# Performance work log

Measured on AMD Instinct MI355X. Metric: run time of the kernel, lower is better.

## Reference

```python
import jax, jax.numpy as jnp
import numpy as np

N, M, D = 500000, 128, 16

def setup_inputs() -> dict:
    key = jax.random.key(0)
    k1, k2, k3 = jax.random.split(key, 3)
    points = jax.random.uniform(k1, (N, D), dtype=jnp.float32)
    centers = jax.random.uniform(k2, (M, D), dtype=jnp.float32)
    # module initializes covs_inv_sqrt = 15*I per center; add small noise so it's non-trivial
    covs_inv_sqrt = 15.0 * jnp.eye(D, dtype=jnp.float32)[None, :, :] \
        + 0.1 * jax.random.normal(k3, (M, D, D), dtype=jnp.float32)
    weights = jnp.ones((M,), dtype=jnp.float32)
    threshold = jnp.zeros((1,), dtype=jnp.float32)
    return {"points": points, "centers": centers, "covs_inv_sqrt": covs_inv_sqrt,
            "weights": weights, "threshold": threshold}

def reference(points, centers, covs_inv_sqrt, weights, threshold):
    # refresh(): covs_inv = L @ L^T per center
    covs_inv = jnp.einsum('jde,jfe->jdf', covs_inv_sqrt, covs_inv_sqrt)  # [M,D,D]
    # equal_clusters=True branch
    w = jnp.abs(weights)
    center_prs = w / (w.sum() + 1e-30)
    coefs = center_prs * jnp.sqrt(jnp.linalg.det(covs_inv))  # [M]
    # Mahalanobis quadratic form (x-c)^T S (x-c) expanded as xSx - 2 xSc + cSc
    S_flat = covs_inv.reshape(M, D * D)                          # [M,D^2]
    xx = (points[:, :, None] * points[:, None, :]).reshape(-1, D * D)  # [N,D^2]
    Sc = jnp.einsum('jde,je->jd', covs_inv, centers)             # [M,D]
    cSc = jnp.einsum('jd,jd->j', centers, Sc)                    # [M]
    q = xx @ S_flat.T - 2.0 * (points @ Sc.T) + cSc[None, :]     # [N,M]
    d_ij = -0.5 * q
    # weighted online logsumexp over centers (KeOps logsumexp with weight Vj(coefs))
    log_lik = jax.nn.logsumexp(d_ij, axis=1, b=coefs[None, :], keepdims=True)  # [N,1]
    return log_lik - threshold
```

## Files before the change

kernel.cpp:

```cpp
#include <hip/hip_runtime.h>
#include <math.h>

#define M_CTR 128
#define D_DIM 16
#define KSTEPS 10
#define NSLOT 80
#define GRID_MAIN 4096
#define WS_CONST_F32_OFF 10240
#define LOG2E 1.4426950408889634f
#define LN2   0.6931471805599453f

typedef _Float16 half8 __attribute__((ext_vector_type(8)));
typedef float f32x16 __attribute__((ext_vector_type(16)));

struct SlotTab { unsigned char a[NSLOT]; unsigned char b[NSLOT]; unsigned char m[NSLOT]; };
constexpr SlotTab make_tab() {
    SlotTab T{};
    int s = 0;
    for (int d = 0; d < 8; ++d) { T.a[s] = (unsigned char)d; T.b[s] = (unsigned char)d; T.m[s] = 0; ++s; }
    for (int d = 0; d < 8; ++d)
        for (int f = d + 1; f < 8; ++f) { T.a[s] = (unsigned char)d; T.b[s] = (unsigned char)f; T.m[s] = 0; ++s; }
    for (int d = 0; d < 8; ++d)
        for (int f2 = d + 1; f2 < 8; ++f2) { T.a[s] = (unsigned char)d; T.b[s] = (unsigned char)(f2 + 8); T.m[s] = 0; ++s; }
    for (int d = 0; d < 4; ++d) { T.a[s] = (unsigned char)d; T.b[s] = (unsigned char)(d + 8); T.m[s] = 1; ++s; }
    for (int d = 0; d < 8; ++d) { T.a[s] = (unsigned char)d; T.b[s] = 0; T.m[s] = 2; ++s; }
    for (; s < NSLOT; ++s) { T.a[s] = 0; T.b[s] = 0; T.m[s] = 3; }
    return T;
}
constexpr SlotTab TAB = make_tab();

__global__ __launch_bounds__(64) void gmm_prep_kernel(
    const float* __restrict__ centers,
    const float* __restrict__ Lmat,
    const float* __restrict__ weights,
    float* __restrict__ ws)
{
    const int j    = blockIdx.x;
    const int lane = threadIdx.x;
    const int r    = lane & 15;

    __shared__ float S_lds[D_DIM][D_DIM + 1];
    __shared__ float Scp_lds[D_DIM];

    float Lr[D_DIM];
    {
        const float4* Lrow = (const float4*)(Lmat + (size_t)j * 256 + r * 16);
        #pragma unroll
        for (int q = 0; q < 4; ++q) {
            const float4 v = Lrow[q];
            Lr[q * 4 + 0] = v.x; Lr[q * 4 + 1] = v.y;
            Lr[q * 4 + 2] = v.z; Lr[q * 4 + 3] = v.w;
        }
    }

    float u[D_DIM];
    #pragma unroll
    for (int e = 0; e < D_DIM; ++e) u[e] = Lr[e];
    float logdet = 0.f;
    #pragma unroll
    for (int k = 0; k < D_DIM; ++k) {
        const float pk = __shfl(u[k], k);
        logdet += logf(fabsf(pk));
        const float f = u[k] * (1.0f / pk);
        #pragma unroll
        for (int c = k + 1; c < D_DIM; ++c) {
            const float rkc = __shfl(u[c], k);
            if (r > k) u[c] -= f * rkc;
        }
    }

    #pragma unroll
    for (int f = 0; f < D_DIM; ++f) {
        float acc = 0.f;
        #pragma unroll
        for (int e = 0; e < D_DIM; ++e) acc += Lr[e] * __shfl(Lr[e], f);
        if (lane < D_DIM) S_lds[lane][f] = acc;
    }
    __syncthreads();

    float c[D_DIM];
    {
        const float4* cc = (const float4*)(centers + (size_t)j * D_DIM);
        #pragma unroll
        for (int q = 0; q < 4; ++q) {
            const float4 v = cc[q];
            c[q * 4 + 0] = v.x - 0.5f; c[q * 4 + 1] = v.y - 0.5f;
            c[q * 4 + 2] = v.z - 0.5f; c[q * 4 + 3] = v.w - 0.5f;
        }
    }
    if (lane < D_DIM) {
        float acc = 0.f;
        #pragma unroll
        for (int f = 0; f < D_DIM; ++f) acc += S_lds[lane][f] * c[f];
        Scp_lds[lane] = acc;
    }
    __syncthreads();
    float cSc = 0.f;
    #pragma unroll
    for (int d = 0; d < D_DIM; ++d) cSc += c[d] * Scp_lds[d];

    float wa = fabsf(weights[lane]) + fabsf(weights[lane + 64]);
    #pragma unroll
    for (int off = 32; off > 0; off >>= 1) wa += __shfl_xor(wa, off);
    const float lc = logf(fabsf(weights[j])) - logf(wa + 1e-30f) + logdet;

    float* constsG = ws + WS_CONST_F32_OFF;
    if (lane == 0) constsG[j] = (lc - 0.5f * cSc) * LOG2E;

    if (lane < 2 * KSTEPS) {
        const int t  = lane >> 1;
        const int hi = lane & 1;
        const int h  = j >> 6;
        const int mt = (j >> 5) & 1;
        half8 hv;
        for (int e = 0; e < 8; ++e) {
            const int s  = t * 8 + e;
            const int mm = TAB.m[s], a = TAB.a[s], b = TAB.b[s];
            float val;
            if (mm == 0) {
                const int d = hi ? ((a + 8) & 15) : a;
                const int f = hi ? ((b + 8) & 15) : b;
                val = (d == f) ? -0.5f * S_lds[d][d] : -S_lds[d][f];
            } else if (mm == 1) {
                const int d = a + 4 * hi, f = a + 8 + 4 * hi;
                val = -S_lds[d][f];
            } else if (mm == 2) {
                val = Scp_lds[a + 8 * hi];
            } else {
                val = 0.f;
            }
            hv[e] = (_Float16)(val * LOG2E);
        }
        char* dst = (char*)ws + ((((h * 2 + mt) * KSTEPS + t) * 64) + hi * 32 + (j & 31)) * 16;
        *(half8*)dst = hv;
    }
}

__global__ __launch_bounds__(128, 2) void gmm_main_kernel(
    const float* __restrict__ points,
    const float* __restrict__ wsf,
    const float* __restrict__ thr,
    float* __restrict__ out,
    int ntiles)
{
    const int tid = threadIdx.x;
    const int w   = tid >> 6;
    const int l   = tid & 63;
    const int col = l & 31;
    const bool hi = (l >> 5) != 0;

    half8 A[2][KSTEPS];
    {
        const char* wsb = (const char*)wsf;
        #pragma unroll
        for (int mt = 0; mt < 2; ++mt)
            #pragma unroll
            for (int t = 0; t < KSTEPS; ++t)
                A[mt][t] = *(const half8*)(wsb + ((((w * 2 + mt) * KSTEPS + t) * 64) + l) * 16);
    }

    float cst[32];
    {
        const float* cstG = wsf + WS_CONST_F32_OFF;
        #pragma unroll
        for (int mt = 0; mt < 2; ++mt)
            #pragma unroll
            for (int rr = 0; rr < 16; ++rr)
                cst[mt * 16 + rr] =
                    cstG[w * 64 + mt * 32 + (rr & 3) + 8 * (rr >> 2) + 4 * (l >> 5)];
    }

    const float thrv = thr[0];
    __shared__ float lm[2][2][32], ls[2][2][32];

    const float4* pbase = (const float4*)points;
    int tile = blockIdx.x;
    int par  = 0;
    float4 pf0, pf1, pf2, pf3;
    if (tile < ntiles) {
        const float4* px = pbase + ((size_t)tile * 32 + col) * 4;
        pf0 = px[0]; pf1 = px[1]; pf2 = px[2]; pf3 = px[3];
    }

    for (; tile < ntiles; tile += GRID_MAIN, par ^= 1) {
        float z[D_DIM];
        z[0]=pf0.x-0.5f; z[1]=pf0.y-0.5f; z[2]=pf0.z-0.5f; z[3]=pf0.w-0.5f;
        z[4]=pf1.x-0.5f; z[5]=pf1.y-0.5f; z[6]=pf1.z-0.5f; z[7]=pf1.w-0.5f;
        z[8]=pf2.x-0.5f; z[9]=pf2.y-0.5f; z[10]=pf2.z-0.5f; z[11]=pf2.w-0.5f;
        z[12]=pf3.x-0.5f; z[13]=pf3.y-0.5f; z[14]=pf3.z-0.5f; z[15]=pf3.w-0.5f;

        float zs8[16], z4l[4], z4h[4];
        #pragma unroll
        for (int i = 0; i < 16; ++i) zs8[i] = hi ? z[(i + 8) & 15] : z[i];
        #pragma unroll
        for (int i = 0; i < 4; ++i) {
            z4l[i] = hi ? z[i + 4]  : z[i];
            z4h[i] = hi ? z[i + 12] : z[i + 8];
        }

        f32x16 acc0 = {0.f, 0.f, 0.f, 0.f, 0.f, 0.f, 0.f, 0.f,
                       0.f, 0.f, 0.f, 0.f, 0.f, 0.f, 0.f, 0.f};
        f32x16 acc1 = acc0;

        #pragma unroll
        for (int t = 0; t < KSTEPS; ++t) {
            half8 bf;
            #pragma unroll
            for (int e = 0; e < 8; ++e) {
                const int s  = t * 8 + e;
                const int mm = TAB.m[s], a = TAB.a[s], b = TAB.b[s];
                float p = (mm == 0) ? zs8[a] * zs8[b]
                        : (mm == 1) ? z4l[a] * z4h[a]
                        : (mm == 2) ? zs8[a]
                        : 0.f;
                bf[e] = (_Float16)p;
            }
            acc0 = __builtin_amdgcn_mfma_f32_32x32x16_f16(A[0][t], bf, acc0, 0, 0, 0);
            acc1 = __builtin_amdgcn_mfma_f32_32x32x16_f16(A[1][t], bf, acc1, 0, 0, 0);
        }

        {
            const int nxt = tile + GRID_MAIN;
            if (nxt < ntiles) {
                const float4* px = pbase + ((size_t)nxt * 32 + col) * 4;
                pf0 = px[0]; pf1 = px[1]; pf2 = px[2]; pf3 = px[3];
            }
        }

        float v[32];
        #pragma unroll
        for (int rr = 0; rr < 16; ++rr) {
            v[rr]      = acc0[rr] + cst[rr];
            v[16 + rr] = acc1[rr] + cst[16 + rr];
        }
        float tm[16];
        #pragma unroll
        for (int i = 0; i < 16; ++i) tm[i] = fmaxf(v[i], v[i + 16]);
        float r0 = fmaxf(fmaxf(tm[0], tm[1]), tm[2]);
        float r1 = fmaxf(fmaxf(tm[3], tm[4]), tm[5]);
        float r2 = fmaxf(fmaxf(tm[6], tm[7]), tm[8]);
        float r3 = fmaxf(fmaxf(tm[9], tm[10]), tm[11]);
        float r4 = fmaxf(fmaxf(tm[12], tm[13]), tm[14]);
        float ra = fmaxf(fmaxf(r0, r1), r2);
        float rb = fmaxf(fmaxf(r3, r4), tm[15]);
        const float mx = fmaxf(ra, rb);

        float s0 = 0.f, s1 = 0.f, s2 = 0.f, s3 = 0.f;
        #pragma unroll
        for (int i = 0; i < 32; i += 4) {
            s0 += __builtin_amdgcn_exp2f(v[i + 0] - mx);
            s1 += __builtin_amdgcn_exp2f(v[i + 1] - mx);
            s2 += __builtin_amdgcn_exp2f(v[i + 2] - mx);
            s3 += __builtin_amdgcn_exp2f(v[i + 3] - mx);
        }
        float ss = (s0 + s1) + (s2 + s3);

        const float om = __shfl_xor(mx, 32);
        const float os = __shfl_xor(ss, 32);
        const float M2 = fmaxf(mx, om);
        const float S2 = ss * __builtin_amdgcn_exp2f(mx - M2)
                       + os * __builtin_amdgcn_exp2f(om - M2);

        if (l < 32) { lm[par][w][l] = M2; ls[par][w][l] = S2; }
        __syncthreads();
        if (w == 0 && l < 32) {
            const float m0 = lm[par][0][l], m1 = lm[par][1][l];
            const float MM = fmaxf(m0, m1);
            const float SS = ls[par][0][l] * __builtin_amdgcn_exp2f(m0 - MM)
                           + ls[par][1][l] * __builtin_amdgcn_exp2f(m1 - MM);
            out[tile * 32 + l] = fmaf(LN2, MM + __builtin_amdgcn_logf(SS), -thrv);
        }
    }
}

extern "C" void kernel_launch(void* const* d_in, const int* in_sizes, int n_in,
                              void* d_out, int out_size, void* d_ws, size_t ws_size,
                              hipStream_t stream) {
    const float* points  = (const float*)d_in[0];
    const float* centers = (const float*)d_in[1];
    const float* covs    = (const float*)d_in[2];
    const float* weights = (const float*)d_in[3];
    const float* thr     = (const float*)d_in[4];
    float* out = (float*)d_out;
    float* ws  = (float*)d_ws;

    const int n      = in_sizes[0] / D_DIM;
    const int ntiles = n / 32;

    gmm_prep_kernel<<<M_CTR, 64, 0, stream>>>(centers, covs, weights, ws);
    gmm_main_kernel<<<GRID_MAIN, 128, 0, stream>>>(points, ws, thr, out, ntiles);
}
```

Before: 46.73 us.

## Give each wave all 128 centers, stage weights in LDS, fold constants into MFMA

```diff
diff --git a/kernel.cpp b/kernel.cpp
--- a/kernel.cpp
+++ b/kernel.cpp
@@ -5,13 +5,13 @@
 #define D_DIM 16
 #define KSTEPS 10
 #define NSLOT 80
-#define GRID_MAIN 4096
-#define WS_CONST_F32_OFF 10240
+#define GRID_MAIN 1024
 #define LOG2E 1.4426950408889634f
 #define LN2   0.6931471805599453f
 
-typedef _Float16 half8 __attribute__((ext_vector_type(8)));
-typedef float f32x16 __attribute__((ext_vector_type(16)));
+typedef _Float16 half8  __attribute__((ext_vector_type(8)));
+typedef __fp16   fp16x2 __attribute__((ext_vector_type(2)));
+typedef float   f32x16  __attribute__((ext_vector_type(16)));
 
 struct SlotTab { unsigned char a[NSLOT]; unsigned char b[NSLOT]; unsigned char m[NSLOT]; };
 constexpr SlotTab make_tab() {
@@ -103,15 +103,12 @@
     #pragma unroll
     for (int off = 32; off > 0; off >>= 1) wa += __shfl_xor(wa, off);
     const float lc = logf(fabsf(weights[j])) - logf(wa + 1e-30f) + logdet;
-
-    float* constsG = ws + WS_CONST_F32_OFF;
-    if (lane == 0) constsG[j] = (lc - 0.5f * cSc) * LOG2E;
+    const float cst_half = (lc - 0.5f * cSc) * 0.5f;
 
     if (lane < 2 * KSTEPS) {
         const int t  = lane >> 1;
         const int hi = lane & 1;
-        const int h  = j >> 6;
-        const int mt = (j >> 5) & 1;
+        const int mt = j >> 5;
         half8 hv;
         for (int e = 0; e < 8; ++e) {
             const int s  = t * 8 + e;
@@ -127,62 +124,53 @@
             } else if (mm == 2) {
                 val = Scp_lds[a + 8 * hi];
             } else {
-                val = 0.f;
+                val = (s == 76) ? cst_half : 0.f;
             }
             hv[e] = (_Float16)(val * LOG2E);
         }
-        char* dst = (char*)ws + ((((h * 2 + mt) * KSTEPS + t) * 64) + hi * 32 + (j & 31)) * 16;
+        char* dst = (char*)ws + (((mt * KSTEPS + t) * 64) + hi * 32 + (j & 31)) * 16;
         *(half8*)dst = hv;
     }
 }
 
-__global__ __launch_bounds__(128, 2) void gmm_main_kernel(
+__global__ __launch_bounds__(256) void gmm_main_kernel(
     const float* __restrict__ points,
     const float* __restrict__ wsf,
     const float* __restrict__ thr,
     float* __restrict__ out,
     int ntiles)
 {
+    __shared__ float4 A_lds4[2560];
+
     const int tid = threadIdx.x;
     const int w   = tid >> 6;
     const int l   = tid & 63;
     const int col = l & 31;
     const bool hi = (l >> 5) != 0;
 
-    half8 A[2][KSTEPS];
     {
-        const char* wsb = (const char*)wsf;
-        #pragma unroll
-        for (int mt = 0; mt < 2; ++mt)
-            #pragma unroll
-            for (int t = 0; t < KSTEPS; ++t)
-                A[mt][t] = *(const half8*)(wsb + ((((w * 2 + mt) * KSTEPS + t) * 64) + l) * 16);
-    }
-
-    float cst[32];
-    {
-        const float* cstG = wsf + WS_CONST_F32_OFF;
-        #pragma unroll
-        for (int mt = 0; mt < 2; ++mt)
-            #pragma unroll
-            for (int rr = 0; rr < 16; ++rr)
-                cst[mt * 16 + rr] =
-                    cstG[w * 64 + mt * 32 + (rr & 3) + 8 * (rr >> 2) + 4 * (l >> 5)];
-    }
-
+        const float4* src = (const float4*)wsf;
+        #pragma unroll
+        for (int i = 0; i < 10; ++i)
+            A_lds4[i * 256 + tid] = src[i * 256 + tid];
+    }
+    __syncthreads();
+
+    const half8* Ah = (const half8*)A_lds4 + l;
     const float thrv = thr[0];
-    __shared__ float lm[2][2][32], ls[2][2][32];
-
     const float4* pbase = (const float4*)points;
-    int tile = blockIdx.x;
-    int par  = 0;
+
+    const int wid    = blockIdx.x * 4 + w;
+    const int stride = GRID_MAIN * 4;
+
+    int tile = wid;
     float4 pf0, pf1, pf2, pf3;
     if (tile < ntiles) {
         const float4* px = pbase + ((size_t)tile * 32 + col) * 4;
         pf0 = px[0]; pf1 = px[1]; pf2 = px[2]; pf3 = px[3];
     }
 
-    for (; tile < ntiles; tile += GRID_MAIN, par ^= 1) {
+    for (; tile < ntiles; tile += stride) {
         float z[D_DIM];
         z[0]=pf0.x-0.5f; z[1]=pf0.y-0.5f; z[2]=pf0.z-0.5f; z[3]=pf0.w-0.5f;
         z[4]=pf1.x-0.5f; z[5]=pf1.y-0.5f; z[6]=pf1.z-0.5f; z[7]=pf1.w-0.5f;
@@ -198,60 +186,64 @@
             z4h[i] = hi ? z[i + 12] : z[i + 8];
         }
 
-        f32x16 acc0 = {0.f, 0.f, 0.f, 0.f, 0.f, 0.f, 0.f, 0.f,
-                       0.f, 0.f, 0.f, 0.f, 0.f, 0.f, 0.f, 0.f};
-        f32x16 acc1 = acc0;
+        f32x16 acc0 = {0.f,0.f,0.f,0.f,0.f,0.f,0.f,0.f,0.f,0.f,0.f,0.f,0.f,0.f,0.f,0.f};
+        f32x16 acc1 = acc0, acc2 = acc0, acc3 = acc0;
 
         #pragma unroll
         for (int t = 0; t < KSTEPS; ++t) {
-            half8 bf;
+            float pv[8];
             #pragma unroll
             for (int e = 0; e < 8; ++e) {
                 const int s  = t * 8 + e;
                 const int mm = TAB.m[s], a = TAB.a[s], b = TAB.b[s];
-                float p = (mm == 0) ? zs8[a] * zs8[b]
-                        : (mm == 1) ? z4l[a] * z4h[a]
-                        : (mm == 2) ? zs8[a]
-                        : 0.f;
-                bf[e] = (_Float16)p;
+                pv[e] = (mm == 0) ? zs8[a] * zs8[b]
+                      : (mm == 1) ? z4l[a] * z4h[a]
+                      : (mm == 2) ? zs8[a]
+                      : ((s == 76) ? 1.0f : 0.0f);
             }
-            acc0 = __builtin_amdgcn_mfma_f32_32x32x16_f16(A[0][t], bf, acc0, 0, 0, 0);
-            acc1 = __builtin_amdgcn_mfma_f32_32x32x16_f16(A[1][t], bf, acc1, 0, 0, 0);
+            union { half8 h8; fp16x2 h2[4]; } u;
+            u.h2[0] = __builtin_amdgcn_cvt_pkrtz(pv[0], pv[1]);
+            u.h2[1] = __builtin_amdgcn_cvt_pkrtz(pv[2], pv[3]);
+            u.h2[2] = __builtin_amdgcn_cvt_pkrtz(pv[4], pv[5]);
+            u.h2[3] = __builtin_amdgcn_cvt_pkrtz(pv[6], pv[7]);
+            const half8 bf = u.h8;
+
+            const half8 a0 = Ah[(0 * KSTEPS + t) * 64];
+            const half8 a1 = Ah[(1 * KSTEPS + t) * 64];
+            const half8 a2 = Ah[(2 * KSTEPS + t) * 64];
+            const half8 a3 = Ah[(3 * KSTEPS + t) * 64];
+            acc0 = __builtin_amdgcn_mfma_f32_32x32x16_f16(a0, bf, acc0, 0, 0, 0);
+            acc1 = __builtin_amdgcn_mfma_f32_32x32x16_f16(a1, bf, acc1, 0, 0, 0);
+            acc2 = __builtin_amdgcn_mfma_f32_32x32x16_f16(a2, bf, acc2, 0, 0, 0);
+            acc3 = __builtin_amdgcn_mfma_f32_32x32x16_f16(a3, bf, acc3, 0, 0, 0);
         }
 
         {
-            const int nxt = tile + GRID_MAIN;
+            const int nxt = tile + stride;
             if (nxt < ntiles) {
                 const float4* px = pbase + ((size_t)nxt * 32 + col) * 4;
                 pf0 = px[0]; pf1 = px[1]; pf2 = px[2]; pf3 = px[3];
             }
         }
 
-        float v[32];
+        float t0[8];
+        #pragma unroll
+        for (int i = 0; i < 8; ++i)
+            t0[i] = fmaxf(fmaxf(acc0[i], acc0[i + 8]), fmaxf(acc1[i], acc1[i + 8]));
+        #pragma unroll
+        for (int i = 0; i < 8; ++i)
+            t0[i] = fmaxf(t0[i], fmaxf(fmaxf(acc2[i], acc2[i + 8]), fmaxf(acc3[i], acc3[i + 8])));
+        float m0 = fmaxf(fmaxf(t0[0], t0[1]), fmaxf(t0[2], t0[3]));
+        float m1 = fmaxf(fmaxf(t0[4], t0[5]), fmaxf(t0[6], t0[7]));
+        const float mx = fmaxf(m0, m1);
+
+        float s0 = 0.f, s1 = 0.f, s2 = 0.f, s3 = 0.f;
         #pragma unroll
         for (int rr = 0; rr < 16; ++rr) {
-            v[rr]      = acc0[rr] + cst[rr];
-            v[16 + rr] = acc1[rr] + cst[16 + rr];
-        }
-        float tm[16];
-        #pragma unroll
-        for (int i = 0; i < 16; ++i) tm[i] = fmaxf(v[i], v[i + 16]);
-        float r0 = fmaxf(fmaxf(tm[0], tm[1]), tm[2]);
-        float r1 = fmaxf(fmaxf(tm[3], tm[4]), tm[5]);
-        float r2 = fmaxf(fmaxf(tm[6], tm[7]), tm[8]);
-        float r3 = fmaxf(fmaxf(tm[9], tm[10]), tm[11]);
-        float r4 = fmaxf(fmaxf(tm[12], tm[13]), tm[14]);
-        float ra = fmaxf(fmaxf(r0, r1), r2);
-        float rb = fmaxf(fmaxf(r3, r4), tm[15]);
-        const float mx = fmaxf(ra, rb);
-
-        float s0 = 0.f, s1 = 0.f, s2 = 0.f, s3 = 0.f;
-        #pragma unroll
-        for (int i = 0; i < 32; i += 4) {
-            s0 += __builtin_amdgcn_exp2f(v[i + 0] - mx);
-            s1 += __builtin_amdgcn_exp2f(v[i + 1] - mx);
-            s2 += __builtin_amdgcn_exp2f(v[i + 2] - mx);
-            s3 += __builtin_amdgcn_exp2f(v[i + 3] - mx);
+            s0 += __builtin_amdgcn_exp2f(acc0[rr] - mx);
+            s1 += __builtin_amdgcn_exp2f(acc1[rr] - mx);
+            s2 += __builtin_amdgcn_exp2f(acc2[rr] - mx);
+            s3 += __builtin_amdgcn_exp2f(acc3[rr] - mx);
         }
         float ss = (s0 + s1) + (s2 + s3);
 
@@ -261,15 +253,8 @@
         const float S2 = ss * __builtin_amdgcn_exp2f(mx - M2)
                        + os * __builtin_amdgcn_exp2f(om - M2);
 
-        if (l < 32) { lm[par][w][l] = M2; ls[par][w][l] = S2; }
-        __syncthreads();
-        if (w == 0 && l < 32) {
-            const float m0 = lm[par][0][l], m1 = lm[par][1][l];
-            const float MM = fmaxf(m0, m1);
-            const float SS = ls[par][0][l] * __builtin_amdgcn_exp2f(m0 - MM)
-                           + ls[par][1][l] * __builtin_amdgcn_exp2f(m1 - MM);
-            out[tile * 32 + l] = fmaf(LN2, MM + __builtin_amdgcn_logf(SS), -thrv);
-        }
+        if (l < 32)
+            out[tile * 32 + l] = fmaf(LN2, M2 + __builtin_amdgcn_logf(S2), -thrv);
     }
 }
 
@@ -288,5 +273,5 @@
     const int ntiles = n / 32;
 
     gmm_prep_kernel<<<M_CTR, 64, 0, stream>>>(centers, covs, weights, ws);
-    gmm_main_kernel<<<GRID_MAIN, 128, 0, stream>>>(points, ws, thr, out, ntiles);
-}
+    gmm_main_kernel<<<GRID_MAIN, 256, 0, stream>>>(points, ws, thr, out, ntiles);
+}
```

Result: faster. 45.51 us (-2.6%).
